# Kernel tuning notes

Measured on AMD Instinct MI355X. Metric: run time of the kernel, lower is better.

## Reference

```python
import jax, jax.numpy as jnp
import numpy as np

PAIR_KEY_BASE = 20000  # token_max + 1
POS_WEIGHT = 1.0
NEG_WEIGHT = 1.0
EPS = 1e-8


def _isin_sorted(x, sorted_keys):
    # torch.isin equivalent given a sorted 1-D key set
    idx = jnp.searchsorted(sorted_keys, x)
    idx = jnp.clip(idx, 0, sorted_keys.shape[0] - 1)
    return sorted_keys[idx] == x


def setup_inputs() -> dict:
    key = jax.random.key(0)
    k_ids, k_tf, k_act, k_prior, k_u, k_v = jax.random.split(key, 6)
    B, S, D, M = 8, 2048, 64, 200000
    input_ids = jax.random.randint(k_ids, (B, S), 0, PAIR_KEY_BASE, dtype=jnp.int32)
    tf_mask = jax.random.randint(k_tf, (B, S), 0, 2) == 1
    active_gene_mask = jax.random.randint(k_act, (B, S), 0, 2) == 1
    # prior GRN pair keys: src*base + tgt, sorted (duplicates are harmless for isin)
    prior_pair_keys = jnp.sort(jax.random.randint(
        k_prior, (M,), 0, PAIR_KEY_BASE * PAIR_KEY_BASE, dtype=jnp.int32))
    # u, v small positive so u @ v^T lands mostly inside (0, 1) before clamping
    u = jax.random.uniform(k_u, (B, S, D), dtype=jnp.float32) * 0.1
    v = jax.random.uniform(k_v, (B, S, D), dtype=jnp.float32) * 0.1
    return {"input_ids": input_ids, "tf_mask": tf_mask,
            "active_gene_mask": active_gene_mask,
            "prior_pair_keys": prior_pair_keys, "u": u, "v": v}


def reference(input_ids, tf_mask, active_gene_mask, prior_pair_keys, u, v):
    # supervise: TF rows x active-gene cols  [B,S,S]
    supervise = tf_mask[:, :, None] & active_gene_mask[:, None, :]
    # pair keys for every (src, tgt) position pair  [B,S,S]
    pair_keys = input_ids[:, :, None] * PAIR_KEY_BASE + input_ids[:, None, :]
    positive = _isin_sorted(pair_keys, prior_pair_keys) & supervise
    target = positive.astype(jnp.float32)
    # edge probabilities, clamped like torch: [B,S,S]
    edge_prob = jnp.clip(jnp.einsum('bsd,btd->bst', u, v), EPS, 1.0 - EPS)
    # binary cross entropy, reduction='none'
    loss = -(target * jnp.log(edge_prob) + (1.0 - target) * jnp.log1p(-edge_prob))
    weight = target * POS_WEIGHT + (1.0 - target) * NEG_WEIGHT
    # neg_sample_ratio=None -> sampled_mask == supervise_mask
    m = supervise.astype(jnp.float32)
    numer = jnp.sum(loss * weight * m)
    denom = jnp.sum(weight * m)
    return numer / (denom + EPS)
```

## Files before the change

### kernel.cpp

```cpp
#include <hip/hip_runtime.h>
#include <math.h>

#define BB 8
#define SS 2048
#define DD 64
#define PAIR_BASE 20000
#define CEPS 1e-8f
#define NROWS (BB * SS)
#define MAIN_BLOCKS (16 * 16 * BB)
#define PPMAX 8192
#define PREP_BLOCKS (1 + BB + BB + BB)

typedef __bf16 bf16x8 __attribute__((ext_vector_type(8)));
typedef __bf16 bf16x4 __attribute__((ext_vector_type(4)));
typedef float  f32x4  __attribute__((ext_vector_type(4)));

struct Ws {
    int byteMode;
    int pad;
    int mc[BB];
    int nc[BB];
    float mpart[MAIN_BLOCKS];
    float ppart[PPMAX];
    int cheadR[BB * PAIR_BASE];
    int cnextR[NROWS];
    int cheadC[BB * PAIR_BASE];
    int cnextC[NROWS];
    __bf16 Uc[(size_t)BB * SS * DD];
    __bf16 Vc[(size_t)BB * SS * DD];
};

__device__ __forceinline__ bool read_mask(const void* p, int i, int byteMode) {
    if (byteMode) return ((const unsigned char*)p)[i] != 0;
    return ((const int*)p)[i] != 0;
}

__device__ __forceinline__ int detect_bm(const void* tf_raw, int tid, int* badl) {
    if (tid == 0) *badl = 0;
    __syncthreads();
    if (((const unsigned int*)tf_raw)[tid] > 1u) atomicOr(badl, 1);
    __syncthreads();
    return *badl;
}

__global__ __launch_bounds__(1024) void prep_kernel(
    const int* __restrict__ ids,
    const void* __restrict__ tf_raw,
    const void* __restrict__ act_raw,
    const float* __restrict__ u,
    const float* __restrict__ v,
    Ws* __restrict__ ws)
{
    __shared__ int badl;
    __shared__ int wsum[16], wbase[16], stot;
    __shared__ unsigned short cidx[SS];

    const int blk = blockIdx.x;
    const int tid = threadIdx.x;
    const int w    = tid >> 6;
    const int lane = tid & 63;

    if (blk == 0) {
        const int bm = detect_bm(tf_raw, tid, &badl);
        if (tid == 0) ws->byteMode = bm;
    } else if (blk <= BB) {
        const int b = blk - 1;
        const int bm = detect_bm(tf_raw, tid, &badl);
        const unsigned long long below = ((unsigned long long)1 << lane) - 1;

        for (int phase = 0; phase < 2; ++phase) {
            const void* mraw = phase ? act_raw : tf_raw;
            const int e0 = b * SS + 2 * tid;
            const int m0 = read_mask(mraw, e0,     bm) ? 1 : 0;
            const int m1 = read_mask(mraw, e0 + 1, bm) ? 1 : 0;
            const unsigned long long k0 = __ballot(m0 != 0);
            const unsigned long long k1 = __ballot(m1 != 0);
            const int exclw = __popcll(k0 & below) + __popcll(k1 & below);
            if (lane == 0) wsum[w] = __popcll(k0) + __popcll(k1);
            __syncthreads();
            if (tid == 0) {
                int run = 0;
                #pragma unroll
                for (int k = 0; k < 16; ++k) { wbase[k] = run; run += wsum[k]; }
                stot = run;
            }
            __syncthreads();
            const int excl = wbase[w] + exclw;
            if (m0) cidx[excl]      = (unsigned short)(2 * tid);
            if (m1) cidx[excl + m0] = (unsigned short)(2 * tid + 1);
            __syncthreads();
            const int total = stot;
            if (tid == 0) { if (phase) ws->nc[b] = total; else ws->mc[b] = total; }
            const int tpad = (total + 127) & ~127;
            __bf16* dst = (phase ? ws->Vc : ws->Uc) + (size_t)b * SS * DD;
            const float* src = (phase ? v : u) + (size_t)b * SS * DD;
            const int r_off = tid >> 4, c = tid & 15;
            for (int r0 = 0; r0 < tpad; r0 += 64) {
                const int r = r0 + r_off;
                if (r < tpad) {
                    bf16x4 hv;
                    if (r < total) {
                        const float4 f = *(const float4*)(src + (size_t)cidx[r] * DD + c * 4);
                        hv = (bf16x4){ (__bf16)f.x, (__bf16)f.y, (__bf16)f.z, (__bf16)f.w };
                    } else {
                        hv = (bf16x4){ (__bf16)0.f, (__bf16)0.f, (__bf16)0.f, (__bf16)0.f };
                    }
                    *(bf16x4*)(dst + (size_t)r * DD + c * 4) = hv;
                }
            }
            __syncthreads();
        }
    } else if (blk <= 2 * BB) {
        const int b = blk - (BB + 1);
        const int bm = detect_bm(tf_raw, tid, &badl);
        int* head = ws->cheadR + b * PAIR_BASE;
        for (int i = tid; i < PAIR_BASE; i += 1024) head[i] = -1;
        __syncthreads();
        for (int s = tid; s < SS; s += 1024) {
            if (read_mask(tf_raw, b * SS + s, bm)) {
                const int id = ids[b * SS + s];
                const int old = atomicExch(&head[id], s);
                ws->cnextR[b * SS + s] = old;
            }
        }
    } else {
        const int b = blk - (2 * BB + 1);
        const int bm = detect_bm(tf_raw, tid, &badl);
        int* head = ws->cheadC + b * PAIR_BASE;
        for (int i = tid; i < PAIR_BASE; i += 1024) head[i] = -1;
        __syncthreads();
        for (int t = tid; t < SS; t += 1024) {
            if (read_mask(act_raw, b * SS + t, bm)) {
                const int id = ids[b * SS + t];
                const int old = atomicExch(&head[id], t);
                ws->cnextC[b * SS + t] = old;
            }
        }
    }
}

__global__ __launch_bounds__(256) void prior_loss_main(Ws* __restrict__ ws)
{
    const int b  = blockIdx.z;
    const int s0 = blockIdx.y * 128;
    const int t0 = blockIdx.x * 128;
    const int tid = threadIdx.x;
    const int flat = (blockIdx.z * gridDim.y + blockIdx.y) * gridDim.x + blockIdx.x;

    const int mcp = (ws->mc[b] + 127) & ~127;
    const int ncp = (ws->nc[b] + 127) & ~127;
    if (s0 >= mcp || t0 >= ncp) {
        if (tid == 0) ws->mpart[flat] = 0.f;
        return;
    }

    __shared__ __align__(16) __bf16 Ulds[128 * 72];
    __shared__ __align__(16) __bf16 Vlds[128 * 72];
    __shared__ float wsumS[4];

    const __bf16* ub = ws->Uc + (size_t)(b * SS + s0) * DD;
    const __bf16* vb = ws->Vc + (size_t)(b * SS + t0) * DD;
    #pragma unroll
    for (int it = 0; it < 4; ++it) {
        int li = tid + it * 256;
        int r  = li >> 3;
        int c8 = li & 7;
        *(bf16x8*)&Ulds[r * 72 + c8 * 8] = *(const bf16x8*)(ub + r * DD + c8 * 8);
        *(bf16x8*)&Vlds[r * 72 + c8 * 8] = *(const bf16x8*)(vb + r * DD + c8 * 8);
    }
    __syncthreads();

    const int w    = tid >> 6;
    const int lane = tid & 63;
    const int quad = lane >> 4;
    const int l15  = lane & 15;
    const int wm0  = (w >> 1) * 64;
    const int wn0  = (w & 1) * 64;

    f32x4 acc[4][4];
    #pragma unroll
    for (int i = 0; i < 4; ++i)
        #pragma unroll
        for (int j = 0; j < 4; ++j)
            acc[i][j] = (f32x4){0.f, 0.f, 0.f, 0.f};

    #pragma unroll
    for (int kh = 0; kh < 2; ++kh) {
        const int kcol = kh * 32 + quad * 8;
        bf16x8 af[4], bfr[4];
        #pragma unroll
        for (int ti = 0; ti < 4; ++ti)
            af[ti] = *(const bf16x8*)&Ulds[(wm0 + ti * 16 + l15) * 72 + kcol];
        #pragma unroll
        for (int tj = 0; tj < 4; ++tj)
            bfr[tj] = *(const bf16x8*)&Vlds[(wn0 + tj * 16 + l15) * 72 + kcol];
        #pragma unroll
        for (int ti = 0; ti < 4; ++ti)
            #pragma unroll
            for (int tj = 0; tj < 4; ++tj)
                acc[ti][tj] = __builtin_amdgcn_mfma_f32_16x16x32_bf16(
                    af[ti], bfr[tj], acc[ti][tj], 0, 0, 0);
    }

    float lsum = 0.f;
    #pragma unroll
    for (int ti = 0; ti < 4; ++ti)
        #pragma unroll
        for (int r = 0; r < 4; ++r)
            #pragma unroll
            for (int tj = 0; tj < 4; ++tj) {
                float q = 1.0f - acc[ti][tj][r];
                q = fminf(fmaxf(q, CEPS), 1.0f - CEPS);
                lsum += __logf(q);
            }
    lsum = -lsum;

    #pragma unroll
    for (int o = 32; o > 0; o >>= 1)
        lsum += __shfl_down(lsum, o, 64);
    if (lane == 0) wsumS[w] = lsum;
    __syncthreads();
    if (tid == 0)
        ws->mpart[flat] = wsumS[0] + wsumS[1] + wsumS[2] + wsumS[3];
}

__global__ __launch_bounds__(256) void positives_kernel(
    const int* __restrict__ prior, int M,
    const float* __restrict__ u,
    const float* __restrict__ v,
    Ws* __restrict__ ws)
{
    __shared__ float wsumS[4];
    const int tid  = threadIdx.x;
    const int w    = tid >> 6;
    const int lane = tid & 63;
    const int b    = blockIdx.y;
    const int i    = blockIdx.x * 256 + tid;

    float corr = 0.f;
    if (i < M) {
        const int key = prior[i];
        const bool dup = (i > 0) && (prior[i - 1] == key);
        if (!dup) {
            const unsigned int uk  = (unsigned int)key;
            const unsigned int src = uk / PAIR_BASE;
            const unsigned int tgt = uk - src * PAIR_BASE;
            int r = ws->cheadR[b * PAIR_BASE + (int)src];
            if (r >= 0) {
                const int* nxtR = ws->cnextR + b * SS;
                const int* nxtC = ws->cnextC + b * SS;
                const int thead = ws->cheadC[b * PAIR_BASE + (int)tgt];
                for (; r >= 0; r = nxtR[r]) {
                    const float* urow = u + (size_t)(b * SS + r) * DD;
                    for (int t = thead; t >= 0; t = nxtC[t]) {
                        const float* vrow = v + (size_t)(b * SS + t) * DD;
                        float dot = 0.f;
                        #pragma unroll
                        for (int k2 = 0; k2 < DD; k2 += 4) {
                            float4 a = *(const float4*)(urow + k2);
                            float4 c = *(const float4*)(vrow + k2);
                            dot += (float)(__bf16)a.x * (float)(__bf16)c.x;
                            dot += (float)(__bf16)a.y * (float)(__bf16)c.y;
                            dot += (float)(__bf16)a.z * (float)(__bf16)c.z;
                            dot += (float)(__bf16)a.w * (float)(__bf16)c.w;
                        }
                        float p = fminf(fmaxf(dot, CEPS), 1.0f - CEPS);
                        float q = fminf(fmaxf(1.0f - dot, CEPS), 1.0f - CEPS);
                        corr += __logf(q) - __logf(p);
                    }
                }
            }
        }
    }

    #pragma unroll
    for (int o = 32; o > 0; o >>= 1)
        corr += __shfl_down(corr, o, 64);
    if (lane == 0) wsumS[w] = corr;
    __syncthreads();
    if (tid == 0)
        ws->ppart[blockIdx.y * gridDim.x + blockIdx.x] =
            wsumS[0] + wsumS[1] + wsumS[2] + wsumS[3];
}

__global__ __launch_bounds__(256) void finalize_kernel(const Ws* __restrict__ ws,
                                                       int npp,
                                                       float* __restrict__ out) {
    __shared__ double sred[256];
    const int tid = threadIdx.x;
    double s = 0.0;
    for (int i = tid; i < MAIN_BLOCKS; i += 256) s += (double)ws->mpart[i];
    for (int i = tid; i < npp;         i += 256) s += (double)ws->ppart[i];
    sred[tid] = s;
    __syncthreads();
    for (int o = 128; o > 0; o >>= 1) {
        if (tid < o) sred[tid] += sred[tid + o];
        __syncthreads();
    }
    if (tid == 0) {
        double denom = 0.0;
        for (int b = 0; b < BB; ++b)
            denom += (double)ws->mc[b] * (double)ws->nc[b];
        out[0] = (float)(sred[0] / (denom + 1e-8));
    }
}

extern "C" void kernel_launch(void* const* d_in, const int* in_sizes, int n_in,
                              void* d_out, int out_size, void* d_ws, size_t ws_size,
                              hipStream_t stream) {
    (void)n_in; (void)out_size; (void)ws_size;
    const int*   ids   = (const int*)d_in[0];
    const void*  tf    = d_in[1];
    const void*  act   = d_in[2];
    const int*   prior = (const int*)d_in[3];
    const int    M     = in_sizes[3];
    const float* u     = (const float*)d_in[4];
    const float* v     = (const float*)d_in[5];
    Ws* ws = (Ws*)d_ws;
    float* out = (float*)d_out;

    prep_kernel<<<PREP_BLOCKS, 1024, 0, stream>>>(ids, tf, act, u, v, ws);
    dim3 grid(16, 16, BB);
    prior_loss_main<<<grid, 256, 0, stream>>>(ws);
    int pbx = (M + 255) / 256;
    if (pbx * BB > PPMAX) pbx = PPMAX / BB;
    dim3 pgrid(pbx, BB);
    positives_kernel<<<pgrid, 256, 0, stream>>>(prior, M, u, v, ws);
    finalize_kernel<<<1, 256, 0, stream>>>(ws, pbx * BB, out);
}
```

Baseline: 126.5 us.

## Split prep gather across slices and merge main/positives into one launch

The prep kernel's compaction and bf16 conversion of u/v rows is spread over 8 slice blocks per batch instead of one, so more CUs share the gather. The dense MFMA tile kernel and the prior-positives correction kernel are merged into one work kernel with a combined grid, which removes a launch and lets the two phases overlap. Each positives thread now loops over all batches for its key, which cuts the positives grid by a factor of 8 but gives each thread more serial work. Each slice block redundantly recomputes the mask prefix scan.

```diff
diff --git a/kernel.cpp b/kernel.cpp
--- a/kernel.cpp
+++ b/kernel.cpp
@@ -8,8 +8,8 @@
 #define CEPS 1e-8f
 #define NROWS (BB * SS)
 #define MAIN_BLOCKS (16 * 16 * BB)
-#define PPMAX 8192
-#define PREP_BLOCKS (1 + BB + BB + BB)
+#define PPMAX 1024
+#define PREP_BLOCKS (64 + BB + BB + 1)
 
 typedef __bf16 bf16x8 __attribute__((ext_vector_type(8)));
 typedef __bf16 bf16x4 __attribute__((ext_vector_type(4)));
@@ -55,16 +55,14 @@
     __shared__ int wsum[16], wbase[16], stot;
     __shared__ unsigned short cidx[SS];
 
-    const int blk = blockIdx.x;
-    const int tid = threadIdx.x;
+    const int blk  = blockIdx.x;
+    const int tid  = threadIdx.x;
     const int w    = tid >> 6;
     const int lane = tid & 63;
 
-    if (blk == 0) {
-        const int bm = detect_bm(tf_raw, tid, &badl);
-        if (tid == 0) ws->byteMode = bm;
-    } else if (blk <= BB) {
-        const int b = blk - 1;
+    if (blk < 64) {
+        const int b     = blk >> 3;
+        const int slice = blk & 7;
         const int bm = detect_bm(tf_raw, tid, &badl);
         const unsigned long long below = ((unsigned long long)1 << lane) - 1;
 
@@ -90,14 +88,19 @@
             if (m1) cidx[excl + m0] = (unsigned short)(2 * tid + 1);
             __syncthreads();
             const int total = stot;
-            if (tid == 0) { if (phase) ws->nc[b] = total; else ws->mc[b] = total; }
+            if (tid == 0 && slice == 0) {
+                if (phase) ws->nc[b] = total; else ws->mc[b] = total;
+            }
             const int tpad = (total + 127) & ~127;
+            const int rbeg = slice * 256;
+            const int rend = min(rbeg + 256, tpad);
             __bf16* dst = (phase ? ws->Vc : ws->Uc) + (size_t)b * SS * DD;
             const float* src = (phase ? v : u) + (size_t)b * SS * DD;
             const int r_off = tid >> 4, c = tid & 15;
-            for (int r0 = 0; r0 < tpad; r0 += 64) {
-                const int r = r0 + r_off;
-                if (r < tpad) {
+            #pragma unroll
+            for (int p4 = 0; p4 < 4; ++p4) {
+                const int r = rbeg + p4 * 64 + r_off;
+                if (r < rend) {
                     bf16x4 hv;
                     if (r < total) {
                         const float4 f = *(const float4*)(src + (size_t)cidx[r] * DD + c * 4);
@@ -110,8 +113,8 @@
             }
             __syncthreads();
         }
-    } else if (blk <= 2 * BB) {
-        const int b = blk - (BB + 1);
+    } else if (blk < 64 + BB) {
+        const int b = blk - 64;
         const int bm = detect_bm(tf_raw, tid, &badl);
         int* head = ws->cheadR + b * PAIR_BASE;
         for (int i = tid; i < PAIR_BASE; i += 1024) head[i] = -1;
@@ -123,8 +126,8 @@
                 ws->cnextR[b * SS + s] = old;
             }
         }
-    } else {
-        const int b = blk - (2 * BB + 1);
+    } else if (blk < 64 + 2 * BB) {
+        const int b = blk - (64 + BB);
         const int bm = detect_bm(tf_raw, tid, &badl);
         int* head = ws->cheadC + b * PAIR_BASE;
         for (int i = tid; i < PAIR_BASE; i += 1024) head[i] = -1;
@@ -136,84 +139,138 @@
                 ws->cnextC[b * SS + t] = old;
             }
         }
+    } else {
+        const int bm = detect_bm(tf_raw, tid, &badl);
+        if (tid == 0) ws->byteMode = bm;
     }
 }
 
-__global__ __launch_bounds__(256) void prior_loss_main(Ws* __restrict__ ws)
+__global__ __launch_bounds__(256) void work_kernel(
+    const int* __restrict__ prior, int M,
+    const float* __restrict__ u,
+    const float* __restrict__ v,
+    Ws* __restrict__ ws)
 {
-    const int b  = blockIdx.z;
-    const int s0 = blockIdx.y * 128;
-    const int t0 = blockIdx.x * 128;
-    const int tid = threadIdx.x;
-    const int flat = (blockIdx.z * gridDim.y + blockIdx.y) * gridDim.x + blockIdx.x;
-
-    const int mcp = (ws->mc[b] + 127) & ~127;
-    const int ncp = (ws->nc[b] + 127) & ~127;
-    if (s0 >= mcp || t0 >= ncp) {
-        if (tid == 0) ws->mpart[flat] = 0.f;
-        return;
-    }
-
     __shared__ __align__(16) __bf16 Ulds[128 * 72];
     __shared__ __align__(16) __bf16 Vlds[128 * 72];
     __shared__ float wsumS[4];
 
-    const __bf16* ub = ws->Uc + (size_t)(b * SS + s0) * DD;
-    const __bf16* vb = ws->Vc + (size_t)(b * SS + t0) * DD;
-    #pragma unroll
-    for (int it = 0; it < 4; ++it) {
-        int li = tid + it * 256;
-        int r  = li >> 3;
-        int c8 = li & 7;
-        *(bf16x8*)&Ulds[r * 72 + c8 * 8] = *(const bf16x8*)(ub + r * DD + c8 * 8);
-        *(bf16x8*)&Vlds[r * 72 + c8 * 8] = *(const bf16x8*)(vb + r * DD + c8 * 8);
-    }
-    __syncthreads();
-
+    const int bid  = blockIdx.x;
+    const int tid  = threadIdx.x;
     const int w    = tid >> 6;
     const int lane = tid & 63;
-    const int quad = lane >> 4;
-    const int l15  = lane & 15;
-    const int wm0  = (w >> 1) * 64;
-    const int wn0  = (w & 1) * 64;
-
-    f32x4 acc[4][4];
-    #pragma unroll
-    for (int i = 0; i < 4; ++i)
-        #pragma unroll
-        for (int j = 0; j < 4; ++j)
-            acc[i][j] = (f32x4){0.f, 0.f, 0.f, 0.f};
-
-    #pragma unroll
-    for (int kh = 0; kh < 2; ++kh) {
-        const int kcol = kh * 32 + quad * 8;
-        bf16x8 af[4], bfr[4];
-        #pragma unroll
-        for (int ti = 0; ti < 4; ++ti)
-            af[ti] = *(const bf16x8*)&Ulds[(wm0 + ti * 16 + l15) * 72 + kcol];
-        #pragma unroll
-        for (int tj = 0; tj < 4; ++tj)
-            bfr[tj] = *(const bf16x8*)&Vlds[(wn0 + tj * 16 + l15) * 72 + kcol];
-        #pragma unroll
-        for (int ti = 0; ti < 4; ++ti)
-            #pragma unroll
-            for (int tj = 0; tj < 4; ++tj)
-                acc[ti][tj] = __builtin_amdgcn_mfma_f32_16x16x32_bf16(
-                    af[ti], bfr[tj], acc[ti][tj], 0, 0, 0);
+
+    float lsum = 0.f;
+    float* slot;
+
+    if (bid < MAIN_BLOCKS) {
+        const int b  = bid >> 8;
+        const int by = (bid >> 4) & 15;
+        const int bx = bid & 15;
+        const int s0 = by * 128;
+        const int t0 = bx * 128;
+        slot = &ws->mpart[bid];
+
+        const int mcp = (ws->mc[b] + 127) & ~127;
+        const int ncp = (ws->nc[b] + 127) & ~127;
+        if (s0 < mcp && t0 < ncp) {
+            const __bf16* ub = ws->Uc + (size_t)(b * SS + s0) * DD;
+            const __bf16* vb = ws->Vc + (size_t)(b * SS + t0) * DD;
+            #pragma unroll
+            for (int it = 0; it < 4; ++it) {
+                int li = tid + it * 256;
+                int r  = li >> 3;
+                int c8 = li & 7;
+                *(bf16x8*)&Ulds[r * 72 + c8 * 8] = *(const bf16x8*)(ub + r * DD + c8 * 8);
+                *(bf16x8*)&Vlds[r * 72 + c8 * 8] = *(const bf16x8*)(vb + r * DD + c8 * 8);
+            }
+            __syncthreads();
+
+            const int quad = lane >> 4;
+            const int l15  = lane & 15;
+            const int wm0  = (w >> 1) * 64;
+            const int wn0  = (w & 1) * 64;
+
+            f32x4 acc[4][4];
+            #pragma unroll
+            for (int i = 0; i < 4; ++i)
+                #pragma unroll
+                for (int j = 0; j < 4; ++j)
+                    acc[i][j] = (f32x4){0.f, 0.f, 0.f, 0.f};
+
+            #pragma unroll
+            for (int kh = 0; kh < 2; ++kh) {
+                const int kcol = kh * 32 + quad * 8;
+                bf16x8 af[4], bfr[4];
+                #pragma unroll
+                for (int ti = 0; ti < 4; ++ti)
+                    af[ti] = *(const bf16x8*)&Ulds[(wm0 + ti * 16 + l15) * 72 + kcol];
+                #pragma unroll
+                for (int tj = 0; tj < 4; ++tj)
+                    bfr[tj] = *(const bf16x8*)&Vlds[(wn0 + tj * 16 + l15) * 72 + kcol];
+                #pragma unroll
+                for (int ti = 0; ti < 4; ++ti)
+                    #pragma unroll
+                    for (int tj = 0; tj < 4; ++tj)
+                        acc[ti][tj] = __builtin_amdgcn_mfma_f32_16x16x32_bf16(
+                            af[ti], bfr[tj], acc[ti][tj], 0, 0, 0);
+            }
+
+            #pragma unroll
+            for (int ti = 0; ti < 4; ++ti)
+                #pragma unroll
+                for (int r = 0; r < 4; ++r)
+                    #pragma unroll
+                    for (int tj = 0; tj < 4; ++tj) {
+                        float q = 1.0f - acc[ti][tj][r];
+                        q = fminf(fmaxf(q, CEPS), 1.0f - CEPS);
+                        lsum += __logf(q);
+                    }
+            lsum = -lsum;
+        }
+    } else {
+        const int pid = bid - MAIN_BLOCKS;
+        const int i   = pid * 256 + tid;
+        slot = &ws->ppart[pid];
+
+        if (i < M) {
+            const int key = prior[i];
+            const bool dup = (i > 0) && (prior[i - 1] == key);
+            if (!dup) {
+                const unsigned int uk  = (unsigned int)key;
+                const unsigned int src = uk / PAIR_BASE;
+                const unsigned int tgt = uk - src * PAIR_BASE;
+                #pragma unroll
+                for (int b = 0; b < BB; ++b) {
+                    int r = ws->cheadR[b * PAIR_BASE + (int)src];
+                    if (r < 0) continue;
+                    const int thead = ws->cheadC[b * PAIR_BASE + (int)tgt];
+                    if (thead < 0) continue;
+                    const int* nxtR = ws->cnextR + b * SS;
+                    const int* nxtC = ws->cnextC + b * SS;
+                    for (; r >= 0; r = nxtR[r]) {
+                        const float* urow = u + (size_t)(b * SS + r) * DD;
+                        for (int t = thead; t >= 0; t = nxtC[t]) {
+                            const float* vrow = v + (size_t)(b * SS + t) * DD;
+                            float dot = 0.f;
+                            #pragma unroll
+                            for (int k2 = 0; k2 < DD; k2 += 4) {
+                                float4 a = *(const float4*)(urow + k2);
+                                float4 c = *(const float4*)(vrow + k2);
+                                dot += (float)(__bf16)a.x * (float)(__bf16)c.x;
+                                dot += (float)(__bf16)a.y * (float)(__bf16)c.y;
+                                dot += (float)(__bf16)a.z * (float)(__bf16)c.z;
+                                dot += (float)(__bf16)a.w * (float)(__bf16)c.w;
+                            }
+                            float p = fminf(fmaxf(dot, CEPS), 1.0f - CEPS);
+                            float q = fminf(fmaxf(1.0f - dot, CEPS), 1.0f - CEPS);
+                            lsum += __logf(q) - __logf(p);
+                        }
+                    }
+                }
+            }
+        }
     }
-
-    float lsum = 0.f;
-    #pragma unroll
-    for (int ti = 0; ti < 4; ++ti)
-        #pragma unroll
-        for (int r = 0; r < 4; ++r)
-            #pragma unroll
-            for (int tj = 0; tj < 4; ++tj) {
-                float q = 1.0f - acc[ti][tj][r];
-                q = fminf(fmaxf(q, CEPS), 1.0f - CEPS);
-                lsum += __logf(q);
-            }
-    lsum = -lsum;
 
     #pragma unroll
     for (int o = 32; o > 0; o >>= 1)
@@ -221,66 +278,7 @@
     if (lane == 0) wsumS[w] = lsum;
     __syncthreads();
     if (tid == 0)
-        ws->mpart[flat] = wsumS[0] + wsumS[1] + wsumS[2] + wsumS[3];
-}
-
-__global__ __launch_bounds__(256) void positives_kernel(
-    const int* __restrict__ prior, int M,
-    const float* __restrict__ u,
-    const float* __restrict__ v,
-    Ws* __restrict__ ws)
-{
-    __shared__ float wsumS[4];
-    const int tid  = threadIdx.x;
-    const int w    = tid >> 6;
-    const int lane = tid & 63;
-    const int b    = blockIdx.y;
-    const int i    = blockIdx.x * 256 + tid;
-
-    float corr = 0.f;
-    if (i < M) {
-        const int key = prior[i];
-        const bool dup = (i > 0) && (prior[i - 1] == key);
-        if (!dup) {
-            const unsigned int uk  = (unsigned int)key;
-            const unsigned int src = uk / PAIR_BASE;
-            const unsigned int tgt = uk - src * PAIR_BASE;
-            int r = ws->cheadR[b * PAIR_BASE + (int)src];
-            if (r >= 0) {
-                const int* nxtR = ws->cnextR + b * SS;
-                const int* nxtC = ws->cnextC + b * SS;
-                const int thead = ws->cheadC[b * PAIR_BASE + (int)tgt];
-                for (; r >= 0; r = nxtR[r]) {
-                    const float* urow = u + (size_t)(b * SS + r) * DD;
-                    for (int t = thead; t >= 0; t = nxtC[t]) {
-                        const float* vrow = v + (size_t)(b * SS + t) * DD;
-                        float dot = 0.f;
-                        #pragma unroll
-                        for (int k2 = 0; k2 < DD; k2 += 4) {
-                            float4 a = *(const float4*)(urow + k2);
-                            float4 c = *(const float4*)(vrow + k2);
-                            dot += (float)(__bf16)a.x * (float)(__bf16)c.x;
-                            dot += (float)(__bf16)a.y * (float)(__bf16)c.y;
-                            dot += (float)(__bf16)a.z * (float)(__bf16)c.z;
-                            dot += (float)(__bf16)a.w * (float)(__bf16)c.w;
-                        }
-                        float p = fminf(fmaxf(dot, CEPS), 1.0f - CEPS);
-                        float q = fminf(fmaxf(1.0f - dot, CEPS), 1.0f - CEPS);
-                        corr += __logf(q) - __logf(p);
-                    }
-                }
-            }
-        }
-    }
-
-    #pragma unroll
-    for (int o = 32; o > 0; o >>= 1)
-        corr += __shfl_down(corr, o, 64);
-    if (lane == 0) wsumS[w] = corr;
-    __syncthreads();
-    if (tid == 0)
-        ws->ppart[blockIdx.y * gridDim.x + blockIdx.x] =
-            wsumS[0] + wsumS[1] + wsumS[2] + wsumS[3];
+        *slot = wsumS[0] + wsumS[1] + wsumS[2] + wsumS[3];
 }
 
 __global__ __launch_bounds__(256) void finalize_kernel(const Ws* __restrict__ ws,
@@ -319,12 +317,10 @@
     Ws* ws = (Ws*)d_ws;
     float* out = (float*)d_out;
 
+    int npos = (M + 255) / 256;
+    if (npos > PPMAX) npos = PPMAX;
+
     prep_kernel<<<PREP_BLOCKS, 1024, 0, stream>>>(ids, tf, act, u, v, ws);
-    dim3 grid(16, 16, BB);
-    prior_loss_main<<<grid, 256, 0, stream>>>(ws);
-    int pbx = (M + 255) / 256;
-    if (pbx * BB > PPMAX) pbx = PPMAX / BB;
-    dim3 pgrid(pbx, BB);
-    positives_kernel<<<pgrid, 256, 0, stream>>>(prior, M, u, v, ws);
-    finalize_kernel<<<1, 256, 0, stream>>>(ws, pbx * BB, out);
-}
+    work_kernel<<<MAIN_BLOCKS + npos, 256, 0, stream>>>(prior, M, u, v, ws);
+    finalize_kernel<<<1, 256, 0, stream>>>(ws, npos, out);
+}
```

Measured after the change: 115.0 us. 1.1x faster.
